# Kernel optimization log

Hardware: AMD Instinct MI355X
Metric: run time of the kernel (lower is better)

## Reference

```python
import jax, jax.numpy as jnp
import numpy as np

NEG_INF = -1e9  # matches tf mask value -1000000000.0
LEAKY_ALPHA = 0.2  # tf.nn.leaky_relu default


def setup_inputs() -> dict:
    key = jax.random.key(0)
    k1, k2, k3, k4 = jax.random.split(key, 4)
    B, N, F, U = 8, 2048, 128, 128
    X = jax.random.normal(k1, (B, N, F), dtype=jnp.float32)
    A = jax.random.randint(k2, (B, N, N), 0, 2, dtype=jnp.int32)
    W = jax.random.normal(k3, (F, U), dtype=jnp.float32) * 0.1
    a = jax.random.normal(k4, (2 * U, 1), dtype=jnp.float32) * 0.1
    return {"X": X, "A": A, "W": W, "a": a}


def reference(X, A, W, a):
    # H = X @ W : [B, N, U]
    H = jnp.einsum('bnf,fu->bnu', X, W)
    U = H.shape[-1]
    # Additive decomposition of the tile+concat: [H_i || H_j] @ a = H_i@a_src + H_j@a_dst
    a_src = a[:U, 0]   # [U]
    a_dst = a[U:, 0]   # [U]
    s = H @ a_src      # [B, N]
    t = H @ a_dst      # [B, N]
    e = s[:, :, None] + t[:, None, :]            # [B, N, N] pairwise logits
    e = jax.nn.leaky_relu(e, negative_slope=LEAKY_ALPHA)
    mask = jnp.where(A > 0, 0.0, NEG_INF).astype(e.dtype)
    attention = jax.nn.softmax(e + mask, axis=-1)  # [B, N, N]
    H_out = jnp.einsum('bij,bju->biu', attention, H)
    return jax.nn.relu(H_out)
```

## Files before the change

### kernel.cpp

```cpp
#include <hip/hip_runtime.h>
#include <hip/hip_bf16.h>


#define NEG_INF -1.0e9f

typedef __bf16 bf16x8 __attribute__((ext_vector_type(8)));
typedef unsigned short ushort8 __attribute__((ext_vector_type(8)));
typedef float f32x4 __attribute__((ext_vector_type(4)));

__device__ __forceinline__ unsigned short f2b(float x) {
    unsigned u = __builtin_bit_cast(unsigned, x);
    u += 0x7fffu + ((u >> 16) & 1u);
    return (unsigned short)(u >> 16);
}

__device__ __forceinline__ void gload_lds16(const void* g, void* l) {
    __builtin_amdgcn_global_load_lds(
        (const __attribute__((address_space(1))) void*)g,
        (__attribute__((address_space(3))) void*)l, 16, 0, 0);
}

__global__ __launch_bounds__(256) void k_wt(const float* __restrict__ W,
                                            unsigned short* __restrict__ WT) {
    int tid = blockIdx.x * 256 + threadIdx.x;
    int u = tid >> 7, f = tid & 127;
    WT[tid] = f2b(W[f * 128 + u]);
}

__global__ __launch_bounds__(256) void k_h(const float* __restrict__ X,
                                           const unsigned short* __restrict__ WT,
                                           const float* __restrict__ a,
                                           unsigned short* __restrict__ HT,
                                           float* __restrict__ sbuf,
                                           float* __restrict__ tbuf) {
    const int tid  = threadIdx.x;
    const int w    = tid >> 6;
    const int lane = tid & 63;
    const int r    = lane & 15;
    const int cg   = lane >> 4;
    const int row0 = blockIdx.x * 64 + w * 16;
    const int b    = row0 >> 11;
    const int n0   = row0 & 2047;
    const int arow = row0 + r;

    f32x4 acc[8] = {};

#pragma unroll
    for (int k0 = 0; k0 < 128; k0 += 32) {
        const float* xp = X + (size_t)arow * 128 + k0 + cg * 8;
        ushort8 xa;
#pragma unroll
        for (int j = 0; j < 8; j++) xa[j] = f2b(xp[j]);
        bf16x8 av = __builtin_bit_cast(bf16x8, xa);
#pragma unroll
        for (int ut = 0; ut < 8; ut++) {
            ushort8 wb = *(const ushort8*)(WT + (size_t)(ut * 16 + r) * 128 + k0 + cg * 8);
            acc[ut] = __builtin_amdgcn_mfma_f32_16x16x32_bf16(
                av, __builtin_bit_cast(bf16x8, wb), acc[ut], 0, 0, 0);
        }
    }

    float sp[4] = {0.f, 0.f, 0.f, 0.f};
    float tp[4] = {0.f, 0.f, 0.f, 0.f};
#pragma unroll
    for (int ut = 0; ut < 8; ut++) {
        int u = ut * 16 + r;
        float as = a[u];
        float ad = a[128 + u];
#pragma unroll
        for (int reg = 0; reg < 4; reg++) {
            float h = acc[ut][reg];
            int nrow = n0 + cg * 4 + reg;
            HT[((size_t)b * 128 + u) * 2048 + nrow] = f2b(h);
            sp[reg] += h * as;
            tp[reg] += h * ad;
        }
    }
#pragma unroll
    for (int msk = 1; msk < 16; msk <<= 1) {
#pragma unroll
        for (int reg = 0; reg < 4; reg++) {
            sp[reg] += __shfl_xor(sp[reg], msk);
            tp[reg] += __shfl_xor(tp[reg], msk);
        }
    }
    if (r == 0) {
#pragma unroll
        for (int reg = 0; reg < 4; reg++) {
            int row = row0 + cg * 4 + reg;
            sbuf[row] = sp[reg];
            tbuf[row] = tp[reg];
        }
    }
}

__global__ __launch_bounds__(512, 4) void k_attn(const int* __restrict__ A,
                                                 const unsigned short* __restrict__ HT,
                                                 const float* __restrict__ sbuf,
                                                 const float* __restrict__ tbuf,
                                                 float* __restrict__ out) {
    __shared__ char smem[65536];
    __shared__ float tS[2048];
    __shared__ float dSm[4][2][16];

    const int tid  = threadIdx.x;
    const int w    = tid >> 6;
    const int lane = tid & 63;
    const int r    = lane & 15;
    const int cg   = lane >> 4;
    const int g    = w & 1;
    const int jq   = w >> 1;
    const int bid  = blockIdx.x;
    const int b    = bid & 7;
    const int it   = bid >> 3;
    const int i0   = it * 32;
    const int rot  = it & 15;

    const int irow = i0 + g * 16 + r;
    const float s_r = sbuf[b * 2048 + irow];
    const unsigned short* Hb = HT + ((size_t)b * 128) * 2048 + jq * 512;

    unsigned int* bitsS = (unsigned int*)smem;
    {
        const int* Abase = A + ((size_t)(b * 2048 + i0 + w * 4)) * 2048;
#pragma unroll
        for (int rr = 0; rr < 4; ++rr) {
            const int* Ap = Abase + rr * 2048 + lane * 32;
            unsigned int word = 0;
#pragma unroll
            for (int kk = 0; kk < 8; ++kk) {
                int4 v = *(const int4*)(Ap + kk * 4);
                word |= (v.x > 0 ? 1u : 0u) << (kk * 4 + 0);
                word |= (v.y > 0 ? 1u : 0u) << (kk * 4 + 1);
                word |= (v.z > 0 ? 1u : 0u) << (kk * 4 + 2);
                word |= (v.w > 0 ? 1u : 0u) << (kk * 4 + 3);
            }
            bitsS[(w * 4 + rr) * 65 + lane] = word;
        }
    }
    *(float4*)(tS + tid * 4) = *(const float4*)(tbuf + b * 2048 + tid * 4);
    __syncthreads();

    unsigned int wordsR[16];
#pragma unroll
    for (int k = 0; k < 16; ++k)
        wordsR[k] = bitsS[(g * 16 + r) * 65 + jq * 16 + ((k + rot) & 15)];
    __syncthreads();

    const int srow = (lane >> 2);
    const int csrc = (lane & 3) ^ ((lane >> 2) & 3) ^ ((lane >> 4) & 3);
    char* const qbase = smem + jq * 16384;
    const unsigned short* src0 = Hb + (size_t)(g * 64 + srow) * 2048 + csrc * 8;
    const int rsl = ((r & 3) ^ ((r >> 2) & 3));

    f32x4 acc[8] = {};
    float den = 0.f;

    {
        const int j0 = rot * 32;
#pragma unroll
        for (int i = 0; i < 4; i++)
            gload_lds16(src0 + (size_t)i * 16 * 2048 + j0,
                        qbase + (g * 4 + i) * 1024);
    }
    __syncthreads();

#pragma unroll
    for (int k = 0; k < 16; ++k) {
        const int p = k & 1;
        if (k < 15) {
            const int kn = (k + 1 + rot) & 15;
            char* dst = qbase + (p ^ 1) * 8192;
#pragma unroll
            for (int i = 0; i < 4; i++)
                gload_lds16(src0 + (size_t)i * 16 * 2048 + kn * 32,
                            dst + (g * 4 + i) * 1024);
        }

        const float* tq = tS + jq * 512 + ((k + rot) & 15) * 32 + cg * 8;
        float4 t0 = *(const float4*)(tq);
        float4 t1 = *(const float4*)(tq + 4);
        float tv[8] = {t0.x, t0.y, t0.z, t0.w, t1.x, t1.y, t1.z, t1.w};
        const unsigned int sh = wordsR[k] >> (cg * 8);
        bf16x8 pa;
#pragma unroll
        for (int jj = 0; jj < 8; jj++) {
            float x = s_r + tv[jj];
            float e = fmaxf(x, 0.2f * x);
            float pp = __expf(e - 16.0f);
            pp = ((sh >> jj) & 1u) ? pp : 0.f;
            den += pp;
            pa[jj] = (__bf16)pp;
        }

        const char* buf = qbase + p * 8192;
#pragma unroll
        for (int ut = 0; ut < 8; ut++) {
            ushort8 hb = *(const ushort8*)(buf + (ut * 16 + r) * 64 +
                                           ((cg ^ rsl) * 16));
            acc[ut] = __builtin_amdgcn_mfma_f32_16x16x32_bf16(
                pa, __builtin_bit_cast(bf16x8, hb), acc[ut], 0, 0, 0);
        }

        __syncthreads();
    }

    den += __shfl_xor(den, 16);
    den += __shfl_xor(den, 32);

    float* accS = (float*)smem;
    if (cg == 0) dSm[jq][g][r] = den;
    if (jq != 0) {
        const int rowIdx = ((jq - 1) * 2 + g) * 16 + cg * 4;
#pragma unroll
        for (int ut = 0; ut < 8; ut++)
#pragma unroll
            for (int reg = 0; reg < 4; reg++)
                accS[(rowIdx + reg) * 132 + ut * 16 + r] = acc[ut][reg];
    }
    __syncthreads();
    if (jq == 0) {
        float dinv[4];
#pragma unroll
        for (int reg = 0; reg < 4; reg++) {
            const int row = cg * 4 + reg;
            dinv[reg] = 1.0f / (dSm[0][g][row] + dSm[1][g][row] +
                                dSm[2][g][row] + dSm[3][g][row]);
        }
#pragma unroll
        for (int ut = 0; ut < 8; ut++) {
#pragma unroll
            for (int reg = 0; reg < 4; reg++) {
                const int lrow = cg * 4 + reg;
                float num = acc[ut][reg]
                          + accS[((0 * 2 + g) * 16 + lrow) * 132 + ut * 16 + r]
                          + accS[((1 * 2 + g) * 16 + lrow) * 132 + ut * 16 + r]
                          + accS[((2 * 2 + g) * 16 + lrow) * 132 + ut * 16 + r];
                float o = fmaxf(num * dinv[reg], 0.f);
                out[((size_t)(b * 2048 + i0 + g * 16 + lrow)) * 128 +
                    ut * 16 + r] = o;
            }
        }
    }
}

extern "C" void kernel_launch(void* const* d_in, const int* in_sizes, int n_in,
                              void* d_out, int out_size, void* d_ws, size_t ws_size,
                              hipStream_t stream) {
    const float* X = (const float*)d_in[0];
    const int*   A = (const int*)d_in[1];
    const float* W = (const float*)d_in[2];
    const float* a = (const float*)d_in[3];
    float* out = (float*)d_out;

    char* ws = (char*)d_ws;
    unsigned short* WT  = (unsigned short*)(ws);
    float*          sb  = (float*)(ws + 32768);
    float*          tb  = (float*)(ws + 98304);
    unsigned short* HT  = (unsigned short*)(ws + 163840);

    k_wt<<<dim3(64), dim3(256), 0, stream>>>(W, WT);
    k_h<<<dim3(256), dim3(256), 0, stream>>>(X, WT, a, HT, sb, tb);
    k_attn<<<dim3(512), dim3(512), 0, stream>>>(A, HT, sb, tb, out);
}
```

Before: 65.38 us.

## Stream adjacency mask per tile with register prefetch instead of LDS bitmask prologue

The upfront pass that read each block's adjacency rows, packed them into bitmasks in shared memory and then unpacked them to registers is removed. Each thread now loads its own int32 mask values for the current tile, prefetched two tiles ahead in a double-buffered register array, so mask traffic overlaps the exp/MFMA loop rather than stalling before it. The single __syncthreads per iteration becomes explicit vmcnt waits plus raw s_barrier and sched_barrier, so the compiler cannot reorder around the hand-counted outstanding loads. In exchange, each thread's mask reads are less coalesced (8 ints per lane per row segment) and correctness now depends on the hand-counted vmcnt values.

```diff
diff --git a/kernel.cpp b/kernel.cpp
--- a/kernel.cpp
+++ b/kernel.cpp
@@ -119,33 +119,7 @@
     const int irow = i0 + g * 16 + r;
     const float s_r = sbuf[b * 2048 + irow];
     const unsigned short* Hb = HT + ((size_t)b * 128) * 2048 + jq * 512;
-
-    unsigned int* bitsS = (unsigned int*)smem;
-    {
-        const int* Abase = A + ((size_t)(b * 2048 + i0 + w * 4)) * 2048;
-#pragma unroll
-        for (int rr = 0; rr < 4; ++rr) {
-            const int* Ap = Abase + rr * 2048 + lane * 32;
-            unsigned int word = 0;
-#pragma unroll
-            for (int kk = 0; kk < 8; ++kk) {
-                int4 v = *(const int4*)(Ap + kk * 4);
-                word |= (v.x > 0 ? 1u : 0u) << (kk * 4 + 0);
-                word |= (v.y > 0 ? 1u : 0u) << (kk * 4 + 1);
-                word |= (v.z > 0 ? 1u : 0u) << (kk * 4 + 2);
-                word |= (v.w > 0 ? 1u : 0u) << (kk * 4 + 3);
-            }
-            bitsS[(w * 4 + rr) * 65 + lane] = word;
-        }
-    }
-    *(float4*)(tS + tid * 4) = *(const float4*)(tbuf + b * 2048 + tid * 4);
-    __syncthreads();
-
-    unsigned int wordsR[16];
-#pragma unroll
-    for (int k = 0; k < 16; ++k)
-        wordsR[k] = bitsS[(g * 16 + r) * 65 + jq * 16 + ((k + rot) & 15)];
-    __syncthreads();
+    const int* Aq = A + ((size_t)(b * 2048 + irow)) * 2048 + jq * 512 + cg * 8;
 
     const int srow = (lane >> 2);
     const int csrc = (lane & 3) ^ ((lane >> 2) & 3) ^ ((lane >> 4) & 3);
@@ -156,8 +130,16 @@
     f32x4 acc[8] = {};
     float den = 0.f;
 
+    *(float4*)(tS + tid * 4) = *(const float4*)(tbuf + b * 2048 + tid * 4);
+
+    int4 aP[2][2];
     {
         const int j0 = rot * 32;
+        const int j1 = ((1 + rot) & 15) * 32;
+        aP[0][0] = *(const int4*)(Aq + j0);
+        aP[0][1] = *(const int4*)(Aq + j0 + 4);
+        aP[1][0] = *(const int4*)(Aq + j1);
+        aP[1][1] = *(const int4*)(Aq + j1 + 4);
 #pragma unroll
         for (int i = 0; i < 4; i++)
             gload_lds16(src0 + (size_t)i * 16 * 2048 + j0,
@@ -168,30 +150,43 @@
 #pragma unroll
     for (int k = 0; k < 16; ++k) {
         const int p = k & 1;
-        if (k < 15) {
-            const int kn = (k + 1 + rot) & 15;
-            char* dst = qbase + (p ^ 1) * 8192;
-#pragma unroll
-            for (int i = 0; i < 4; i++)
-                gload_lds16(src0 + (size_t)i * 16 * 2048 + kn * 32,
-                            dst + (g * 4 + i) * 1024);
-        }
 
         const float* tq = tS + jq * 512 + ((k + rot) & 15) * 32 + cg * 8;
         float4 t0 = *(const float4*)(tq);
         float4 t1 = *(const float4*)(tq + 4);
         float tv[8] = {t0.x, t0.y, t0.z, t0.w, t1.x, t1.y, t1.z, t1.w};
-        const unsigned int sh = wordsR[k] >> (cg * 8);
+        int4 ca = aP[k & 1][0], cb = aP[k & 1][1];
+        int ai[8] = {ca.x, ca.y, ca.z, ca.w, cb.x, cb.y, cb.z, cb.w};
         bf16x8 pa;
 #pragma unroll
         for (int jj = 0; jj < 8; jj++) {
             float x = s_r + tv[jj];
             float e = fmaxf(x, 0.2f * x);
             float pp = __expf(e - 16.0f);
-            pp = ((sh >> jj) & 1u) ? pp : 0.f;
+            pp = ai[jj] > 0 ? pp : 0.f;
             den += pp;
             pa[jj] = (__bf16)pp;
         }
+
+        if (k < 14) {
+            const int ja = ((k + 2 + rot) & 15) * 32;
+            aP[k & 1][0] = *(const int4*)(Aq + ja);
+            aP[k & 1][1] = *(const int4*)(Aq + ja + 4);
+        }
+        if (k < 15) {
+            const int jn = ((k + 1 + rot) & 15) * 32;
+            char* dst = qbase + (p ^ 1) * 8192;
+#pragma unroll
+            for (int i = 0; i < 4; i++)
+                gload_lds16(src0 + (size_t)i * 16 * 2048 + jn * 1,
+                            dst + (g * 4 + i) * 1024);
+        }
+
+        if (k < 14)      asm volatile("s_waitcnt vmcnt(6)" ::: "memory");
+        else if (k < 15) asm volatile("s_waitcnt vmcnt(4)" ::: "memory");
+        else             asm volatile("s_waitcnt vmcnt(0)" ::: "memory");
+        __builtin_amdgcn_s_barrier();
+        __builtin_amdgcn_sched_barrier(0);
 
         const char* buf = qbase + p * 8192;
 #pragma unroll
@@ -202,7 +197,8 @@
                 pa, __builtin_bit_cast(bf16x8, hb), acc[ut], 0, 0, 0);
         }
 
-        __syncthreads();
+        __builtin_amdgcn_s_barrier();
+        __builtin_amdgcn_sched_barrier(0);
     }
 
     den += __shfl_xor(den, 16);
```

Result: faster. 59.64 us (-8.8%).
